# Optimization experiments

Hardware: AMD Instinct MI355X
Metric: run time of the kernel (lower is better)

## Reference

```python
import jax, jax.numpy as jnp
import numpy as np

N = 100000   # nodes
E = 1600000  # edges (avg degree 16)
IN, HID, OUT = 128, 128, 64


def _glorot(key, shape):
    limit = np.sqrt(6.0 / (shape[0] + shape[1])).astype(np.float32)
    return jax.random.uniform(key, shape, jnp.float32, -limit, limit)


def setup_inputs() -> dict:
    key = jax.random.key(0)
    ks = jax.random.split(key, 12)
    inp = {}
    for i, (f, s, d) in enumerate([("feat1", "src1", "dst1"), ("feat2", "src2", "dst2"), ("feat", "src", "dst")]):
        inp[f] = jax.random.normal(ks[3 * i], (N, IN), jnp.float32)
        inp[s] = jax.random.randint(ks[3 * i + 1], (E,), 0, N, jnp.int32)
        inp[d] = jax.random.randint(ks[3 * i + 2], (E,), 0, N, jnp.int32)
    inp["W1"] = _glorot(ks[9], (IN, HID))
    inp["b1"] = jnp.zeros((HID,), jnp.float32)
    inp["W2"] = _glorot(ks[10], (HID, OUT))
    inp["b2"] = jnp.zeros((OUT,), jnp.float32)
    return inp


def _gcn_layer(x, src, dst, W, b):
    # DGL GraphConv norm='both': D_dst^{-1/2} * A * D_src^{-1/2} * X * W + b
    ones = jnp.ones(src.shape, jnp.float32)
    deg_out = jax.ops.segment_sum(ones, src, num_segments=N)
    deg_in = jax.ops.segment_sum(ones, dst, num_segments=N)
    norm_src = jax.lax.rsqrt(jnp.maximum(deg_out, 1.0))
    norm_dst = jax.lax.rsqrt(jnp.maximum(deg_in, 1.0))
    h = (x @ W) * norm_src[:, None]           # transform then normalize (math-equivalent order)
    agg = jax.ops.segment_sum(h[src], dst, num_segments=N)  # spmm aggregate
    return agg * norm_dst[:, None] + b


def _encoder(x, src, dst, W1, b1, W2, b2):
    h = jax.nn.relu(_gcn_layer(x, src, dst, W1, b1))
    return _gcn_layer(h, src, dst, W2, b2)


def reference(feat1, src1, dst1, feat2, src2, dst2, feat, src, dst, W1, b1, W2, b2):
    z1 = _encoder(feat1, src1, dst1, W1, b1, W2, b2)
    z2 = _encoder(feat2, src2, dst2, W1, b1, W2, b2)
    z = _encoder(feat, src, dst, W1, b1, W2, b2)
    return (z1, z2, z)
```

## Files before the change

kernel.cpp:

```cpp
#include <hip/hip_runtime.h>

#define NNODES 100000
#define NEDGES 1600000
#define FIN 128
#define FHID 128
#define FOUT 64

typedef unsigned short u16;
typedef unsigned char u8;
typedef unsigned int u32;
typedef __attribute__((ext_vector_type(8))) short short8;
typedef __attribute__((ext_vector_type(4))) float floatx4;

#define NBUK 391
#define NPAD2 (NBUK * 256)
#define NSL2 250
#define SLICE2 (NEDGES / NSL2)
#define SP ((size_t)NSL2 * NBUK)
#define NH16 ((size_t)NNODES * FHID)

__device__ __forceinline__ u16 f2bf(float f) {
  u32 u = __float_as_uint(f);
  u32 r = (u + 0x7fffu + ((u >> 16) & 1u)) >> 16;
  return (u16)r;
}

__device__ __forceinline__ const int* sel(const int* a, const int* b, const int* c, int z) {
  return z == 0 ? a : (z == 1 ? b : c);
}


__global__ __launch_bounds__(256) void bucket_hist_kernel(
    const int* s0, const int* s1, const int* s2,
    const int* d0, const int* d1, const int* d2,
    u16* __restrict__ Hbase, int E) {
  const int z = blockIdx.z;
  const int* __restrict__ src = sel(s0, s1, s2, z);
  const int* __restrict__ dst = sel(d0, d1, d2, z);
  u32* __restrict__ part = (u32*)(Hbase + (size_t)z * NH16);
  u32* __restrict__ part_src = part + SP;
  __shared__ u32 hd[NBUK], hs[NBUK];
  const int s = blockIdx.x;
  for (int i = threadIdx.x; i < NBUK; i += 256) { hd[i] = 0; hs[i] = 0; }
  __syncthreads();
  const int e0 = s * SLICE2, e1 = min(e0 + SLICE2, E);
  const int i0 = e0 >> 2, i1 = e1 >> 2;
  for (int i = i0 + threadIdx.x; i < i1; i += 256) {
    int4 dv = ((const int4*)dst)[i];
    int4 sv = ((const int4*)src)[i];
    atomicAdd(&hd[(u32)dv.x >> 8], 1u);
    atomicAdd(&hd[(u32)dv.y >> 8], 1u);
    atomicAdd(&hd[(u32)dv.z >> 8], 1u);
    atomicAdd(&hd[(u32)dv.w >> 8], 1u);
    atomicAdd(&hs[(u32)sv.x >> 8], 1u);
    atomicAdd(&hs[(u32)sv.y >> 8], 1u);
    atomicAdd(&hs[(u32)sv.z >> 8], 1u);
    atomicAdd(&hs[(u32)sv.w >> 8], 1u);
  }
  __syncthreads();
  for (int i = threadIdx.x; i < NBUK; i += 256) {
    part[(size_t)s * NBUK + i] = hd[i];
    part_src[(size_t)s * NBUK + i] = hs[i];
  }
}

__global__ __launch_bounds__(512) void scan_part_kernel(u16* __restrict__ Hbase,
                                                        u32* __restrict__ boff_d,
                                                        u32* __restrict__ bcount_d,
                                                        u32* __restrict__ boff_s,
                                                        u32* __restrict__ bcount_s) {
  const int z = blockIdx.z;
  u32* base = (u32*)(Hbase + (size_t)z * NH16);
  u32* __restrict__ part = blockIdx.x ? base + SP : base;
  u32* __restrict__ boff = (blockIdx.x ? boff_s : boff_d) + (size_t)z * NBUK;
  u32* __restrict__ bcount = (blockIdx.x ? bcount_s : bcount_d) + (size_t)z * NBUK;
  const int b = threadIdx.x;
  u32 run = 0;
  if (b < NBUK) {
#pragma unroll 5
    for (int s = 0; s < NSL2; s++) {
      u32 v = part[(size_t)s * NBUK + b];
      part[(size_t)s * NBUK + b] = run;
      run += v;
    }
  }
  __shared__ u32 sh[512];
  sh[threadIdx.x] = (b < NBUK) ? run : 0;
  __syncthreads();
  for (int d = 1; d < 512; d <<= 1) {
    u32 t = (threadIdx.x >= d) ? sh[threadIdx.x - d] : 0;
    __syncthreads();
    sh[threadIdx.x] += t;
    __syncthreads();
  }
  if (b < NBUK) {
    boff[b] = sh[threadIdx.x] - run;
    bcount[b] = run;
  }
}

__global__ __launch_bounds__(256) void scatter_kernel(
    const int* s0, const int* s1, const int* s2,
    const int* d0, const int* d1, const int* d2,
    u16* __restrict__ Hbase, u16* __restrict__ Tbase,
    const u32* __restrict__ boff_d, const u32* __restrict__ boff_src, int E) {
  const int z = blockIdx.z;
  const int* __restrict__ src = sel(s0, s1, s2, z);
  const int* __restrict__ dst = sel(d0, d1, d2, z);
  const u32* __restrict__ part = (const u32*)(Hbase + (size_t)z * NH16);
  const u32* __restrict__ part_src = part + SP;
  u8* __restrict__ pes = (u8*)(part_src + SP);
  u32* __restrict__ pe = (u32*)(Tbase + (size_t)z * NH16);
  const u32* __restrict__ boff = boff_d + (size_t)z * NBUK;
  const u32* __restrict__ boff_s = boff_src + (size_t)z * NBUK;
  __shared__ u32 cur[NBUK], curs[NBUK];
  const int s = blockIdx.x;
  for (int i = threadIdx.x; i < NBUK; i += 256) {
    cur[i] = part[(size_t)s * NBUK + i] + boff[i];
    curs[i] = part_src[(size_t)s * NBUK + i] + boff_s[i];
  }
  __syncthreads();
  const int e0 = s * SLICE2, e1 = min(e0 + SLICE2, E);
  const int i0 = e0 >> 2, i1 = e1 >> 2;
  for (int i = i0 + threadIdx.x; i < i1; i += 256) {
    int4 sv = ((const int4*)src)[i];
    int4 dv = ((const int4*)dst)[i];
    u32 p;
    p = atomicAdd(&cur[(u32)dv.x >> 8], 1u); pe[p] = ((u32)sv.x << 8) | ((u32)dv.x & 255u);
    p = atomicAdd(&cur[(u32)dv.y >> 8], 1u); pe[p] = ((u32)sv.y << 8) | ((u32)dv.y & 255u);
    p = atomicAdd(&cur[(u32)dv.z >> 8], 1u); pe[p] = ((u32)sv.z << 8) | ((u32)dv.z & 255u);
    p = atomicAdd(&cur[(u32)dv.w >> 8], 1u); pe[p] = ((u32)sv.w << 8) | ((u32)dv.w & 255u);
    p = atomicAdd(&curs[(u32)sv.x >> 8], 1u); pes[p] = (u8)((u32)sv.x & 255u);
    p = atomicAdd(&curs[(u32)sv.y >> 8], 1u); pes[p] = (u8)((u32)sv.y & 255u);
    p = atomicAdd(&curs[(u32)sv.z >> 8], 1u); pes[p] = (u8)((u32)sv.z & 255u);
    p = atomicAdd(&curs[(u32)sv.w >> 8], 1u); pes[p] = (u8)((u32)sv.w & 255u);
  }
}

__global__ __launch_bounds__(256) void bucket_finish_kernel(
    const u16* __restrict__ Tbase, const u16* __restrict__ Hbase,
    const u32* __restrict__ boffb, const u32* __restrict__ bcountb,
    const u32* __restrict__ boff_sb, const u32* __restrict__ bcount_sb,
    int* __restrict__ csrb, int* __restrict__ offsb, int* __restrict__ degb,
    float* __restrict__ ndb, float* __restrict__ nsb, int* __restrict__ permb, int n) {
  const int z = blockIdx.z;
  const int b = blockIdx.x;
  const int t = threadIdx.x;
  if (blockIdx.y == 1) {
    const u32* partb = (const u32*)(Hbase + (size_t)z * NH16);
    const u8* __restrict__ pes = (const u8*)(partb + 2 * SP);
    const u32* boff = boff_sb + (size_t)z * NBUK;
    const u32* bcount = bcount_sb + (size_t)z * NBUK;
    float* __restrict__ norm_src = nsb + (size_t)z * NNODES;
    const int beg = (int)boff[b];
    const int cnt = (int)bcount[b];
    __shared__ int hh[256];
    hh[t] = 0;
    __syncthreads();
    for (int i = t; i < cnt; i += 256) atomicAdd(&hh[pes[beg + i]], 1);
    __syncthreads();
    const int node = b * 256 + t;
    if (node < n) norm_src[node] = rsqrtf(fmaxf((float)hh[t], 1.0f));
    return;
  }
  const u32* __restrict__ pe = (const u32*)(Tbase + (size_t)z * NH16);
  int* __restrict__ csr = csrb + (size_t)z * NEDGES;
  int* __restrict__ offs = offsb + (size_t)z * NNODES;
  int* __restrict__ deg_dst = degb + (size_t)z * NNODES;
  float* __restrict__ norm_dst = ndb + (size_t)z * NNODES;
  int* __restrict__ perm = permb + (size_t)z * NPAD2;
  const u32* boff = boffb + (size_t)z * NBUK;
  const u32* bcount = bcountb + (size_t)z * NBUK;
  const int beg = (int)boff[b];
  const int cnt = (int)bcount[b];
  __shared__ int h[256], loc[256];
  h[t] = 0;
  __syncthreads();
  for (int i = t; i < cnt; i += 256) atomicAdd(&h[pe[beg + i] & 255u], 1);
  __syncthreads();
  const int myc = h[t];
  loc[t] = myc;
  __syncthreads();
  for (int d = 1; d < 256; d <<= 1) {
    int v = (t >= d) ? loc[t - d] : 0;
    __syncthreads();
    loc[t] += v;
    __syncthreads();
  }
  const int start = beg + loc[t] - myc;
  const int node = b * 256 + t;
  if (node < n) {
    offs[node] = start;
    deg_dst[node] = myc;
    norm_dst[node] = rsqrtf(fmaxf((float)myc, 1.0f));
  }
  __shared__ int dh[64], dbase[64], cnt2[64];
  const int dg = myc > 63 ? 63 : myc;
  if (t < 64) { dh[t] = 0; cnt2[t] = 0; }
  __syncthreads();
  atomicAdd(&dh[dg], 1);
  __syncthreads();
  if (t < 64) dbase[t] = dh[t];
  __syncthreads();
  for (int d = 1; d < 64; d <<= 1) {
    int v = (t >= d && t < 64) ? dbase[t - d] : 0;
    __syncthreads();
    if (t < 64) dbase[t] += v;
    __syncthreads();
  }
  const int rank = dbase[dg] - dh[dg] + atomicAdd(&cnt2[dg], 1);
  perm[b * 256 + rank] = node;
  __syncthreads();
  h[t] = start;
  __syncthreads();
  for (int i = t; i < cnt; i += 256) {
    u32 v = pe[beg + i];
    int p = atomicAdd(&h[v & 255u], 1);
    csr[p] = (int)(v >> 8);
  }
}


#define XP 136

template <int CTOT, bool IN_BF16>
__global__ __launch_bounds__(256) void gemm_mfma(const void* X0, const void* X1,
                                                 const void* X2,
                                                 const float* __restrict__ W,
                                                 const float* __restrict__ normb,
                                                 u16* __restrict__ Yb, int nrows) {
  const int z = blockIdx.z;
  const void* __restrict__ Xv = z == 0 ? X0 : (z == 1 ? X1 : X2);
  const float* __restrict__ norm = normb + (size_t)z * NNODES;
  u16* __restrict__ Y = Yb + (size_t)z * NNODES * CTOT;
  __shared__ u16 Xs[64 * XP];
  __shared__ u16 Wt[64 * XP];
  __shared__ float norm_s[64];
  const int tid = threadIdx.x;
  const int row0 = blockIdx.x * 64;
  const int col0 = blockIdx.y * 64;

  if constexpr (IN_BF16) {
    const u16* X = (const u16*)Xv;
    for (int i = tid; i < 64 * 16; i += 256) {
      int r = i >> 4, k8 = (i & 15) * 8;
      int gr = row0 + r;
      uint4 v = make_uint4(0u, 0u, 0u, 0u);
      if (gr < nrows) v = *(const uint4*)&X[(size_t)gr * 128 + k8];
      *(uint4*)&Xs[r * XP + k8] = v;
    }
  } else {
    const float* X = (const float*)Xv;
    for (int i = tid; i < 64 * 32; i += 256) {
      int r = i >> 5, k4 = (i & 31) * 4;
      int gr = row0 + r;
      ushort4 o = make_ushort4(0, 0, 0, 0);
      if (gr < nrows) {
        float4 v = *(const float4*)&X[(size_t)gr * 128 + k4];
        o.x = f2bf(v.x); o.y = f2bf(v.y); o.z = f2bf(v.z); o.w = f2bf(v.w);
      }
      *(ushort4*)&Xs[r * XP + k4] = o;
    }
  }
  for (int i = tid; i < 128 * 16; i += 256) {
    int k = i >> 4, c4 = (i & 15) * 4;
    float4 v = *(const float4*)&W[(size_t)k * CTOT + col0 + c4];
    Wt[(c4 + 0) * XP + k] = f2bf(v.x);
    Wt[(c4 + 1) * XP + k] = f2bf(v.y);
    Wt[(c4 + 2) * XP + k] = f2bf(v.z);
    Wt[(c4 + 3) * XP + k] = f2bf(v.w);
  }
  if (tid < 64) norm_s[tid] = (row0 + tid < nrows) ? norm[row0 + tid] : 0.f;
  __syncthreads();

  const int w = tid >> 6, lane = tid & 63;
  const int quad = lane >> 4, r16 = lane & 15;
  const int arow = w * 16 + r16;

  short8 a[4];
#pragma unroll
  for (int kc = 0; kc < 4; kc++)
    a[kc] = *(const short8*)&Xs[arow * XP + kc * 32 + quad * 8];

#pragma unroll
  for (int nc = 0; nc < 4; nc++) {
    floatx4 acc = {0.f, 0.f, 0.f, 0.f};
#pragma unroll
    for (int kc = 0; kc < 4; kc++) {
      short8 b = *(const short8*)&Wt[(nc * 16 + r16) * XP + kc * 32 + quad * 8];
      acc = __builtin_amdgcn_mfma_f32_16x16x32_bf16(a[kc], b, acc, 0, 0, 0);
    }
#pragma unroll
    for (int i = 0; i < 4; i++) {
      int lr = w * 16 + quad * 4 + i;
      int gr = row0 + lr;
      if (gr < nrows)
        Y[(size_t)gr * CTOT + col0 + nc * 16 + r16] = f2bf(acc[i] * norm_s[lr]);
    }
  }
}


__device__ __forceinline__ void acc_row(float* acc, uint4 p) {
  acc[0] += __uint_as_float(p.x << 16);
  acc[1] += __uint_as_float(p.x & 0xffff0000u);
  acc[2] += __uint_as_float(p.y << 16);
  acc[3] += __uint_as_float(p.y & 0xffff0000u);
  acc[4] += __uint_as_float(p.z << 16);
  acc[5] += __uint_as_float(p.z & 0xffff0000u);
  acc[6] += __uint_as_float(p.w << 16);
  acc[7] += __uint_as_float(p.w & 0xffff0000u);
}

template <int F, bool RELU, bool OUT_BF16>
__global__ __launch_bounds__(256) void spmm_bf16(const u16* __restrict__ Hbase,
                                                 const int* __restrict__ offsb,
                                                 const int* __restrict__ degb,
                                                 const int* __restrict__ csrb,
                                                 const float* __restrict__ ndb,
                                                 const float* __restrict__ bias,
                                                 const int* __restrict__ permb,
                                                 void* __restrict__ Yv, int n) {
  const int z = blockIdx.z;
  const u16* __restrict__ Hb = Hbase + (size_t)z * NNODES * F;
  const int* __restrict__ offs = offsb + (size_t)z * NNODES;
  const int* __restrict__ deg = degb + (size_t)z * NNODES;
  const int* __restrict__ csr = csrb + (size_t)z * NEDGES;
  const float* __restrict__ norm_dst = ndb + (size_t)z * NNODES;
  const int* __restrict__ perm = permb + (size_t)z * NPAD2;
  constexpr int TPN = F / 8;
  constexpr int NPB = 256 / TPN;
  int idx = blockIdx.x * NPB + threadIdx.x / TPN;
  if (idx >= NPAD2) return;
  int node = perm[idx];
  if (node >= n) return;
  int f0 = (threadIdx.x % TPN) * 8;
  int beg = offs[node];
  int end = beg + deg[node];
  const u16* __restrict__ Hp = Hb + f0;
  float acc[8] = {};
  int e = beg;
  int nfull = (end - beg) >> 2;
  if (nfull > 0) {
    int sv[4]; uint4 p[4];
#pragma unroll
    for (int j = 0; j < 4; j++) sv[j] = csr[e + j];
#pragma unroll
    for (int j = 0; j < 4; j++) p[j] = *(const uint4*)&Hp[(size_t)sv[j] * F];
    for (int b = 1; b < nfull; b++) {
      e += 4;
      int s2[4]; uint4 q[4];
#pragma unroll
      for (int j = 0; j < 4; j++) s2[j] = csr[e + j];
#pragma unroll
      for (int j = 0; j < 4; j++) q[j] = *(const uint4*)&Hp[(size_t)s2[j] * F];
#pragma unroll
      for (int j = 0; j < 4; j++) acc_row(acc, p[j]);
#pragma unroll
      for (int j = 0; j < 4; j++) p[j] = q[j];
    }
#pragma unroll
    for (int j = 0; j < 4; j++) acc_row(acc, p[j]);
    e += 4;
  }
  for (; e < end; e++) {
    int s = csr[e];
    uint4 p = *(const uint4*)&Hp[(size_t)s * F];
    acc_row(acc, p);
  }
  float nd = norm_dst[node];
  float o[8];
#pragma unroll
  for (int i = 0; i < 8; i++) {
    o[i] = fmaf(acc[i], nd, bias[f0 + i]);
    if (RELU) o[i] = fmaxf(o[i], 0.f);
  }
  if constexpr (OUT_BF16) {
    u16* Y = (u16*)Yv + (size_t)z * NNODES * F;
    uint4 pk;
    pk.x = (u32)f2bf(o[0]) | ((u32)f2bf(o[1]) << 16);
    pk.y = (u32)f2bf(o[2]) | ((u32)f2bf(o[3]) << 16);
    pk.z = (u32)f2bf(o[4]) | ((u32)f2bf(o[5]) << 16);
    pk.w = (u32)f2bf(o[6]) | ((u32)f2bf(o[7]) << 16);
    *(uint4*)&Y[(size_t)node * F + f0] = pk;
  } else {
    float* Y = (float*)Yv + (size_t)z * NNODES * F;
    *(float4*)&Y[(size_t)node * F + f0] = make_float4(o[0], o[1], o[2], o[3]);
    *(float4*)&Y[(size_t)node * F + f0 + 4] = make_float4(o[4], o[5], o[6], o[7]);
  }
}


extern "C" void kernel_launch(void* const* d_in, const int* in_sizes, int n_in,
                              void* d_out, int out_size, void* d_ws, size_t ws_size,
                              hipStream_t stream) {
  const int N = NNODES;
  const int E = NEDGES;
  const float* W1 = (const float*)d_in[9];
  const float* b1 = (const float*)d_in[10];
  const float* W2 = (const float*)d_in[11];
  const float* b2 = (const float*)d_in[12];

  const size_t HBYTES = NH16 * 2;

  auto need_for = [&](size_t NG) -> size_t {
    size_t o = 0;
    auto al = [&](size_t b) { o = (o + b + 255) & ~(size_t)255; };
    al(NG * N * 4);
    al(NG * N * 4);
    al(NG * N * 4);
    al(NG * N * 4);
    al(NG * NBUK * 4);
    al(NG * NBUK * 4);
    al(NG * NBUK * 4);
    al(NG * NBUK * 4);
    al(NG * (size_t)NPAD2 * 4);
    al(NG * (size_t)E * 4);
    al(NG * HBYTES);
    al(NG * HBYTES);
    return o;
  };
  const bool batched = ws_size >= need_for(3);
  const size_t NG = batched ? 3 : 1;

  char* ws = (char*)d_ws;
  size_t off = 0;
  auto alloc = [&](size_t bytes) -> void* {
    void* p = ws + off;
    off += (bytes + 255) & ~(size_t)255;
    return p;
  };
  int* deg_dst = (int*)alloc(NG * N * 4);
  float* norm_src = (float*)alloc(NG * N * 4);
  float* norm_dst = (float*)alloc(NG * N * 4);
  int* offs = (int*)alloc(NG * N * 4);
  u32* boff = (u32*)alloc(NG * NBUK * 4);
  u32* bcount = (u32*)alloc(NG * NBUK * 4);
  u32* boff_s = (u32*)alloc(NG * NBUK * 4);
  u32* bcount_s = (u32*)alloc(NG * NBUK * 4);
  int* perm = (int*)alloc(NG * (size_t)NPAD2 * 4);
  int* csr = (int*)alloc(NG * (size_t)E * 4);
  u16* H = (u16*)alloc(NG * HBYTES);
  u16* T = (u16*)alloc(NG * HBYTES);

  const int gemm_rb = (N + 63) / 64;
  const int nb1 = NPAD2 / 16;
  const int nb2 = NPAD2 / 32;

  auto run = [&](const int* s0, const int* s1, const int* s2,
                 const int* d0, const int* d1, const int* d2,
                 const float* f0, const float* f1, const float* f2,
                 const void* x20, const void* x21, const void* x22,
                 void* zoutv, unsigned gz) {
    bucket_hist_kernel<<<dim3(NSL2, 1, gz), 256, 0, stream>>>(s0, s1, s2, d0, d1, d2, H, E);
    scan_part_kernel<<<dim3(2, 1, gz), 512, 0, stream>>>(H, boff, bcount, boff_s, bcount_s);
    scatter_kernel<<<dim3(NSL2, 1, gz), 256, 0, stream>>>(s0, s1, s2, d0, d1, d2,
                                                          H, T, boff, boff_s, E);
    bucket_finish_kernel<<<dim3(NBUK, 2, gz), 256, 0, stream>>>(
        T, H, boff, bcount, boff_s, bcount_s, csr, offs, deg_dst, norm_dst,
        norm_src, perm, N);
    gemm_mfma<FHID, false><<<dim3(gemm_rb, FHID / 64, gz), 256, 0, stream>>>(
        f0, f1, f2, W1, norm_src, H, N);
    spmm_bf16<FHID, true, true><<<dim3(nb1, 1, gz), 256, 0, stream>>>(
        H, offs, deg_dst, csr, norm_dst, b1, perm, T, N);
    gemm_mfma<FOUT, true><<<dim3(gemm_rb, FOUT / 64, gz), 256, 0, stream>>>(
        x20, x21, x22, W2, norm_src, H, N);
    spmm_bf16<FOUT, false, false><<<dim3(nb2, 1, gz), 256, 0, stream>>>(
        H, offs, deg_dst, csr, norm_dst, b2, perm, d_out ? zoutv : zoutv, N);
  };

  if (batched) {
    run((const int*)d_in[1], (const int*)d_in[4], (const int*)d_in[7],
        (const int*)d_in[2], (const int*)d_in[5], (const int*)d_in[8],
        (const float*)d_in[0], (const float*)d_in[3], (const float*)d_in[6],
        T, T + NH16, T + 2 * NH16,
        d_out, 3);
  } else {
    for (int g = 0; g < 3; g++) {
      const float* feat = (const float*)d_in[3 * g + 0];
      const int* src = (const int*)d_in[3 * g + 1];
      const int* dst = (const int*)d_in[3 * g + 2];
      float* zout = (float*)d_out + (size_t)g * N * FOUT;
      run(src, src, src, dst, dst, dst, feat, feat, feat, T, T, T, zout, 1);
    }
  }
}
```

Baseline: 768.0 us.

## Fuse layer-1 SpMM with layer-2 GEMM and drop degree-sorted node permutation

Replaces the separate layer-1 aggregation kernel and the layer-2 GEMM with one kernel. Each block gathers and aggregates 64 nodes' 128-wide features into shared memory, applies bias and ReLU, then runs the MFMA multiply by W2 directly. This avoids writing and re-reading the bf16 hidden activations and saves a launch. It also removes the degree-bucketed node permutation, so aggregation now walks nodes in natural order. That drops the perm construction work but may leave wave load balance worse, and the fused kernel uses only 16 threads per node, which reduces gather parallelism.

```diff
diff --git a/kernel.cpp b/kernel.cpp
--- a/kernel.cpp
+++ b/kernel.cpp
@@ -13,7 +13,6 @@
 typedef __attribute__((ext_vector_type(4))) float floatx4;
 
 #define NBUK 391
-#define NPAD2 (NBUK * 256)
 #define NSL2 250
 #define SLICE2 (NEDGES / NSL2)
 #define SP ((size_t)NSL2 * NBUK)
@@ -142,7 +141,7 @@
     const u32* __restrict__ boffb, const u32* __restrict__ bcountb,
     const u32* __restrict__ boff_sb, const u32* __restrict__ bcount_sb,
     int* __restrict__ csrb, int* __restrict__ offsb, int* __restrict__ degb,
-    float* __restrict__ ndb, float* __restrict__ nsb, int* __restrict__ permb, int n) {
+    float* __restrict__ ndb, float* __restrict__ nsb, int n) {
   const int z = blockIdx.z;
   const int b = blockIdx.x;
   const int t = threadIdx.x;
@@ -168,7 +167,6 @@
   int* __restrict__ offs = offsb + (size_t)z * NNODES;
   int* __restrict__ deg_dst = degb + (size_t)z * NNODES;
   float* __restrict__ norm_dst = ndb + (size_t)z * NNODES;
-  int* __restrict__ perm = permb + (size_t)z * NPAD2;
   const u32* boff = boffb + (size_t)z * NBUK;
   const u32* bcount = bcountb + (size_t)z * NBUK;
   const int beg = (int)boff[b];
@@ -194,22 +192,6 @@
     deg_dst[node] = myc;
     norm_dst[node] = rsqrtf(fmaxf((float)myc, 1.0f));
   }
-  __shared__ int dh[64], dbase[64], cnt2[64];
-  const int dg = myc > 63 ? 63 : myc;
-  if (t < 64) { dh[t] = 0; cnt2[t] = 0; }
-  __syncthreads();
-  atomicAdd(&dh[dg], 1);
-  __syncthreads();
-  if (t < 64) dbase[t] = dh[t];
-  __syncthreads();
-  for (int d = 1; d < 64; d <<= 1) {
-    int v = (t >= d && t < 64) ? dbase[t - d] : 0;
-    __syncthreads();
-    if (t < 64) dbase[t] += v;
-    __syncthreads();
-  }
-  const int rank = dbase[dg] - dh[dg] + atomicAdd(&cnt2[dg], 1);
-  perm[b * 256 + rank] = node;
   __syncthreads();
   h[t] = start;
   __syncthreads();
@@ -232,7 +214,7 @@
   const int z = blockIdx.z;
   const void* __restrict__ Xv = z == 0 ? X0 : (z == 1 ? X1 : X2);
   const float* __restrict__ norm = normb + (size_t)z * NNODES;
-  u16* __restrict__ Y = Yb + (size_t)z * NNODES * CTOT;
+  u16* __restrict__ Y = Yb + (size_t)z * NH16;
   __shared__ u16 Xs[64 * XP];
   __shared__ u16 Wt[64 * XP];
   __shared__ float norm_s[64];
@@ -312,6 +294,125 @@
   acc[7] += __uint_as_float(p.w & 0xffff0000u);
 }
 
+template <int F>
+__device__ __forceinline__ void gather_acc(const u16* __restrict__ Hp,
+                                           const int* __restrict__ csr,
+                                           int beg, int end, float* acc) {
+  int e = beg;
+  int nfull = (end - beg) >> 2;
+  if (nfull > 0) {
+    int sv[4]; uint4 p[4];
+#pragma unroll
+    for (int j = 0; j < 4; j++) sv[j] = csr[e + j];
+#pragma unroll
+    for (int j = 0; j < 4; j++) p[j] = *(const uint4*)&Hp[(size_t)sv[j] * F];
+    for (int b = 1; b < nfull; b++) {
+      e += 4;
+      int s2[4]; uint4 q[4];
+#pragma unroll
+      for (int j = 0; j < 4; j++) s2[j] = csr[e + j];
+#pragma unroll
+      for (int j = 0; j < 4; j++) q[j] = *(const uint4*)&Hp[(size_t)s2[j] * F];
+#pragma unroll
+      for (int j = 0; j < 4; j++) acc_row(acc, p[j]);
+#pragma unroll
+      for (int j = 0; j < 4; j++) p[j] = q[j];
+    }
+#pragma unroll
+    for (int j = 0; j < 4; j++) acc_row(acc, p[j]);
+    e += 4;
+  }
+  for (; e < end; e++) {
+    uint4 p = *(const uint4*)&Hp[(size_t)csr[e] * F];
+    acc_row(acc, p);
+  }
+}
+
+
+__global__ __launch_bounds__(256) void spmm1_gemm2_kernel(
+    const u16* __restrict__ Hbase,
+    const int* __restrict__ offsb, const int* __restrict__ degb,
+    const int* __restrict__ csrb,
+    const float* __restrict__ ndb, const float* __restrict__ b1,
+    const float* __restrict__ W2, const float* __restrict__ nsb,
+    u16* __restrict__ H2base, int n) {
+  const int z = blockIdx.z;
+  const u16* __restrict__ Hb = Hbase + (size_t)z * NH16;
+  const int* __restrict__ offs = offsb + (size_t)z * NNODES;
+  const int* __restrict__ deg = degb + (size_t)z * NNODES;
+  const int* __restrict__ csr = csrb + (size_t)z * NEDGES;
+  const float* __restrict__ nd = ndb + (size_t)z * NNODES;
+  const float* __restrict__ ns = nsb + (size_t)z * NNODES;
+  u16* __restrict__ H2 = H2base + (size_t)z * NH16;
+
+  __shared__ u16 Ts[64 * XP];
+  __shared__ u16 Wt[64 * XP];
+  __shared__ float norm_s[64];
+  const int tid = threadIdx.x;
+  const int row0 = blockIdx.x * 64;
+
+  for (int i = tid; i < 128 * 16; i += 256) {
+    int k = i >> 4, c4 = (i & 15) * 4;
+    float4 v = *(const float4*)&W2[(size_t)k * FOUT + c4];
+    Wt[(c4 + 0) * XP + k] = f2bf(v.x);
+    Wt[(c4 + 1) * XP + k] = f2bf(v.y);
+    Wt[(c4 + 2) * XP + k] = f2bf(v.z);
+    Wt[(c4 + 3) * XP + k] = f2bf(v.w);
+  }
+  if (tid < 64) norm_s[tid] = (row0 + tid < n) ? ns[row0 + tid] : 0.f;
+
+  const int nsub = tid >> 4;
+  const int f0 = (tid & 15) * 8;
+  const u16* __restrict__ Hp = Hb + f0;
+#pragma unroll
+  for (int g = 0; g < 4; g++) {
+    int r = g * 16 + nsub;
+    int node = row0 + r;
+    uint4 pk = make_uint4(0u, 0u, 0u, 0u);
+    if (node < n) {
+      float acc[8] = {};
+      int beg = offs[node];
+      gather_acc<FHID>(Hp, csr, beg, beg + deg[node], acc);
+      float ndv = nd[node];
+      float o[8];
+#pragma unroll
+      for (int i = 0; i < 8; i++)
+        o[i] = fmaxf(fmaf(acc[i], ndv, b1[f0 + i]), 0.f);
+      pk.x = (u32)f2bf(o[0]) | ((u32)f2bf(o[1]) << 16);
+      pk.y = (u32)f2bf(o[2]) | ((u32)f2bf(o[3]) << 16);
+      pk.z = (u32)f2bf(o[4]) | ((u32)f2bf(o[5]) << 16);
+      pk.w = (u32)f2bf(o[6]) | ((u32)f2bf(o[7]) << 16);
+    }
+    *(uint4*)&Ts[r * XP + f0] = pk;
+  }
+  __syncthreads();
+
+  const int w = tid >> 6, lane = tid & 63;
+  const int quad = lane >> 4, r16 = lane & 15;
+  const int arow = w * 16 + r16;
+  short8 a[4];
+#pragma unroll
+  for (int kc = 0; kc < 4; kc++)
+    a[kc] = *(const short8*)&Ts[arow * XP + kc * 32 + quad * 8];
+#pragma unroll
+  for (int nc = 0; nc < 4; nc++) {
+    floatx4 acc = {0.f, 0.f, 0.f, 0.f};
+#pragma unroll
+    for (int kc = 0; kc < 4; kc++) {
+      short8 b = *(const short8*)&Wt[(nc * 16 + r16) * XP + kc * 32 + quad * 8];
+      acc = __builtin_amdgcn_mfma_f32_16x16x32_bf16(a[kc], b, acc, 0, 0, 0);
+    }
+#pragma unroll
+    for (int i = 0; i < 4; i++) {
+      int lr = w * 16 + quad * 4 + i;
+      int gr = row0 + lr;
+      if (gr < n)
+        H2[(size_t)gr * FOUT + nc * 16 + r16] = f2bf(acc[i] * norm_s[lr]);
+    }
+  }
+}
+
+
 template <int F, bool RELU, bool OUT_BF16>
 __global__ __launch_bounds__(256) void spmm_bf16(const u16* __restrict__ Hbase,
                                                  const int* __restrict__ offsb,
@@ -319,55 +420,21 @@
                                                  const int* __restrict__ csrb,
                                                  const float* __restrict__ ndb,
                                                  const float* __restrict__ bias,
-                                                 const int* __restrict__ permb,
                                                  void* __restrict__ Yv, int n) {
   const int z = blockIdx.z;
-  const u16* __restrict__ Hb = Hbase + (size_t)z * NNODES * F;
+  const u16* __restrict__ Hb = Hbase + (size_t)z * NH16;
   const int* __restrict__ offs = offsb + (size_t)z * NNODES;
   const int* __restrict__ deg = degb + (size_t)z * NNODES;
   const int* __restrict__ csr = csrb + (size_t)z * NEDGES;
   const float* __restrict__ norm_dst = ndb + (size_t)z * NNODES;
-  const int* __restrict__ perm = permb + (size_t)z * NPAD2;
   constexpr int TPN = F / 8;
   constexpr int NPB = 256 / TPN;
-  int idx = blockIdx.x * NPB + threadIdx.x / TPN;
-  if (idx >= NPAD2) return;
-  int node = perm[idx];
+  int node = blockIdx.x * NPB + threadIdx.x / TPN;
   if (node >= n) return;
   int f0 = (threadIdx.x % TPN) * 8;
   int beg = offs[node];
-  int end = beg + deg[node];
-  const u16* __restrict__ Hp = Hb + f0;
   float acc[8] = {};
-  int e = beg;
-  int nfull = (end - beg) >> 2;
-  if (nfull > 0) {
-    int sv[4]; uint4 p[4];
-#pragma unroll
-    for (int j = 0; j < 4; j++) sv[j] = csr[e + j];
-#pragma unroll
-    for (int j = 0; j < 4; j++) p[j] = *(const uint4*)&Hp[(size_t)sv[j] * F];
-    for (int b = 1; b < nfull; b++) {
-      e += 4;
-      int s2[4]; uint4 q[4];
-#pragma unroll
-      for (int j = 0; j < 4; j++) s2[j] = csr[e + j];
-#pragma unroll
-      for (int j = 0; j < 4; j++) q[j] = *(const uint4*)&Hp[(size_t)s2[j] * F];
-#pragma unroll
-      for (int j = 0; j < 4; j++) acc_row(acc, p[j]);
-#pragma unroll
-      for (int j = 0; j < 4; j++) p[j] = q[j];
-    }
-#pragma unroll
-    for (int j = 0; j < 4; j++) acc_row(acc, p[j]);
-    e += 4;
-  }
-  for (; e < end; e++) {
-    int s = csr[e];
-    uint4 p = *(const uint4*)&Hp[(size_t)s * F];
-    acc_row(acc, p);
-  }
+  gather_acc<F>(Hb + f0, csr, beg, beg + deg[node], acc);
   float nd = norm_dst[node];
   float o[8];
 #pragma unroll
@@ -414,7 +481,6 @@
     al(NG * NBUK * 4);
     al(NG * NBUK * 4);
     al(NG * NBUK * 4);
-    al(NG * (size_t)NPAD2 * 4);
     al(NG * (size_t)E * 4);
     al(NG * HBYTES);
     al(NG * HBYTES);
@@ -438,19 +504,16 @@
   u32* bcount = (u32*)alloc(NG * NBUK * 4);
   u32* boff_s = (u32*)alloc(NG * NBUK * 4);
   u32* bcount_s = (u32*)alloc(NG * NBUK * 4);
-  int* perm = (int*)alloc(NG * (size_t)NPAD2 * 4);
   int* csr = (int*)alloc(NG * (size_t)E * 4);
   u16* H = (u16*)alloc(NG * HBYTES);
   u16* T = (u16*)alloc(NG * HBYTES);
 
   const int gemm_rb = (N + 63) / 64;
-  const int nb1 = NPAD2 / 16;
-  const int nb2 = NPAD2 / 32;
+  const int nb2 = (N + 31) / 32;
 
   auto run = [&](const int* s0, const int* s1, const int* s2,
                  const int* d0, const int* d1, const int* d2,
                  const float* f0, const float* f1, const float* f2,
-                 const void* x20, const void* x21, const void* x22,
                  void* zoutv, unsigned gz) {
     bucket_hist_kernel<<<dim3(NSL2, 1, gz), 256, 0, stream>>>(s0, s1, s2, d0, d1, d2, H, E);
     scan_part_kernel<<<dim3(2, 1, gz), 512, 0, stream>>>(H, boff, bcount, boff_s, bcount_s);
@@ -458,22 +521,19 @@
                                                           H, T, boff, boff_s, E);
     bucket_finish_kernel<<<dim3(NBUK, 2, gz), 256, 0, stream>>>(
         T, H, boff, bcount, boff_s, bcount_s, csr, offs, deg_dst, norm_dst,
-        norm_src, perm, N);
+        norm_src, N);
     gemm_mfma<FHID, false><<<dim3(gemm_rb, FHID / 64, gz), 256, 0, stream>>>(
         f0, f1, f2, W1, norm_src, H, N);
-    spmm_bf16<FHID, true, true><<<dim3(nb1, 1, gz), 256, 0, stream>>>(
-        H, offs, deg_dst, csr, norm_dst, b1, perm, T, N);
-    gemm_mfma<FOUT, true><<<dim3(gemm_rb, FOUT / 64, gz), 256, 0, stream>>>(
-        x20, x21, x22, W2, norm_src, H, N);
+    spmm1_gemm2_kernel<<<dim3(gemm_rb, 1, gz), 256, 0, stream>>>(
+        H, offs, deg_dst, csr, norm_dst, b1, W2, norm_src, T, N);
     spmm_bf16<FOUT, false, false><<<dim3(nb2, 1, gz), 256, 0, stream>>>(
-        H, offs, deg_dst, csr, norm_dst, b2, perm, d_out ? zoutv : zoutv, N);
+        T, offs, deg_dst, csr, norm_dst, b2, zoutv, N);
   };
 
   if (batched) {
     run((const int*)d_in[1], (const int*)d_in[4], (const int*)d_in[7],
         (const int*)d_in[2], (const int*)d_in[5], (const int*)d_in[8],
         (const float*)d_in[0], (const float*)d_in[3], (const float*)d_in[6],
-        T, T + NH16, T + 2 * NH16,
         d_out, 3);
   } else {
     for (int g = 0; g < 3; g++) {
@@ -481,7 +541,7 @@
       const int* src = (const int*)d_in[3 * g + 1];
       const int* dst = (const int*)d_in[3 * g + 2];
       float* zout = (float*)d_out + (size_t)g * N * FOUT;
-      run(src, src, src, dst, dst, dst, feat, feat, feat, T, T, T, zout, 1);
-    }
-  }
-}
+      run(src, src, src, dst, dst, dst, feat, feat, feat, zout, 1);
+    }
+  }
+}
```

Result: faster. 698.5 us (-9.1%).
